# Optimization experiments

Hardware: AMD Instinct MI355X
Metric: run time of the kernel (lower is better)

Reference implementation:

```python
import jax, jax.numpy as jnp
import numpy as np

M0 = 0.5
M_MIN = 0.25
SCALE = 32.0
NUM_CLASSES = 100000
FEAT_DIM = 256
BATCH = 512


def setup_inputs() -> dict:
    key = jax.random.key(0)
    k1, k2, k3, k4 = jax.random.split(key, 4)
    features = jax.random.normal(k1, (BATCH, FEAT_DIM), dtype=jnp.float32)
    labels = jax.random.randint(k2, (BATCH,), 0, NUM_CLASSES, dtype=jnp.int64)
    weights = jax.random.uniform(k3, (BATCH,), dtype=jnp.float32)
    # xavier_uniform for (num_classes, feat_dim)
    limit = float(np.sqrt(6.0 / (NUM_CLASSES + FEAT_DIM)))
    weight = jax.random.uniform(k4, (NUM_CLASSES, FEAT_DIM), dtype=jnp.float32,
                                minval=-limit, maxval=limit)
    return {"features": features, "weight": weight, "weights": weights, "labels": labels}


def reference(features, weight, weights, labels):
    B = features.shape[0]
    norms = jnp.linalg.norm(features, axis=1)  # (B,)
    lo = jax.lax.stop_gradient(norms.min())
    hi = jax.lax.stop_gradient(norms.max())
    denom = jnp.maximum(hi - lo, 1e-8)
    margins = jnp.clip(M_MIN + (M0 - M_MIN) * (norms - lo) / denom, M_MIN, M0)  # (B,)

    feat_n = features / jnp.maximum(norms, 1e-12)[:, None]
    w_n = weight / jnp.maximum(jnp.linalg.norm(weight, axis=1), 1e-12)[:, None]
    cosine = jnp.clip(feat_n @ w_n.T, -1.0 + 1e-7, 1.0 - 1e-7)  # (B, C)

    rows = jnp.arange(B)
    cos_t = cosine[rows, labels]                      # target cosine (B,)
    theta_t = jnp.arccos(cos_t)
    cos_m_t = cos_t * jnp.cos(margins) - jnp.sin(theta_t) * jnp.sin(margins)

    logits = SCALE * cosine
    logits = logits.at[rows, labels].set(SCALE * cos_m_t)

    logp = jax.nn.log_softmax(logits, axis=1)
    per_sample = -logp[rows, labels]
    return (per_sample * weights).mean()
```

## Files before the change

kernel.cpp:

```cpp
#include <hip/hip_runtime.h>
#include <hip/hip_bf16.h>
#include <math.h>

#define BATCH 512
#define FEAT  256
#define NCLS  100000
#define SCALE_ 32.0f
#define M0_    0.5f
#define MMIN_  0.25f

#define BN 64
#define NT64 1563
#define NSLOTS 256
#define NPART 256
#define K4CHUNK 16
#define NK4 (NPART / K4CHUNK)

#define LOG2E_ 1.44269504088896f
#define K2C_   (SCALE_ * LOG2E_)

typedef unsigned short u16;
typedef short s16x8 __attribute__((ext_vector_type(8)));
typedef float f32x4 __attribute__((ext_vector_type(4)));

__device__ u16   g_fbf16[BATCH * FEAT];
__device__ float g_norms[BATCH];
__device__ float g_dot[BATCH];
__device__ float g_wn2[BATCH];
__device__ float g_psum[NPART * BATCH];
__device__ float g_qs[NK4 * BATCH];
__device__ int   g_lab32;

__device__ __forceinline__ u16 f2b(float x) {
  union { float f; unsigned u; } v; v.f = x;
  unsigned r = v.u + 0x7FFFu + ((v.u >> 16) & 1u);
  return (u16)(r >> 16);
}

__device__ __forceinline__ unsigned pkbf16(float a, float b) {
  unsigned r;
  asm("v_cvt_pk_bf16_f32 %0, %1, %2" : "=v"(r) : "v"(a), "v"(b));
  return r;
}

__device__ __forceinline__ float ex2(float x) {
  return __builtin_amdgcn_exp2f(x);
}

__global__ void k1a(const float* __restrict__ feat, const int* __restrict__ labw) {
  int wid = threadIdx.x >> 6, lane = threadIdx.x & 63;
  int row = blockIdx.x * 4 + wid;
  float4 f = ((const float4*)(feat + row * FEAT))[lane];
  float ss = f.x * f.x + f.y * f.y + f.z * f.z + f.w * f.w;
  #pragma unroll
  for (int d = 1; d < 64; d <<= 1) ss += __shfl_xor(ss, d, 64);
  float nrm = sqrtf(ss);
  float inv = 1.0f / fmaxf(nrm, 1e-12f);
  ushort4 h;
  h.x = f2b(f.x * inv); h.y = f2b(f.y * inv);
  h.z = f2b(f.z * inv); h.w = f2b(f.w * inv);
  ((ushort4*)(g_fbf16 + row * FEAT))[lane] = h;
  if (lane == 0) g_norms[row] = nrm;
  if (blockIdx.x == 0 && wid == 0) {
    int odd = 0;
    #pragma unroll
    for (int k = 0; k < 4; ++k) odd |= labw[2 * (k * 64 + lane) + 1];
    unsigned long long b = __ballot(odd != 0);
    if (lane == 0) g_lab32 = (b != 0ULL) ? 1 : 0;
  }
}

__global__ void k2c(const float* __restrict__ feat, const float* __restrict__ wmat,
                    const void* __restrict__ labels) {
  int wid = threadIdx.x >> 6, lane = threadIdx.x & 63;
  int i = blockIdx.x * 4 + wid;
  long long lab;
  if (g_lab32) lab = (long long)((const int*)labels)[i];
  else         lab = ((const long long*)labels)[i];
  float4 a = ((const float4*)(feat + i * FEAT))[lane];
  float4 b = ((const float4*)(wmat + (size_t)lab * FEAT))[lane];
  float d  = a.x * b.x + a.y * b.y + a.z * b.z + a.w * b.w;
  float bb = b.x * b.x + b.y * b.y + b.z * b.z + b.w * b.w;
  #pragma unroll
  for (int t = 1; t < 64; t <<= 1) {
    d  += __shfl_xor(d, t, 64);
    bb += __shfl_xor(bb, t, 64);
  }
  if (lane == 0) { g_dot[i] = d; g_wn2[i] = bb; }
}


#define LOADC(RB, TILE) do {                                                \
    rowL_ = (RB) + (tid >> 4);                                              \
    int rg_ = (TILE) * BN + rowL_; rg_ = rg_ < NCLS ? rg_ : NCLS - 1;       \
    const float4* src_ = (const float4*)(wmat + (size_t)rg_ * FEAT) + (tid & 15); \
    v_[0] = src_[0]; v_[1] = src_[16]; v_[2] = src_[32]; v_[3] = src_[48];  \
  } while (0)

#define FINISHC(NB) do {                                                    \
    float ss_ = 0.0f;                                                       \
    _Pragma("unroll")                                                       \
    for (int k_ = 0; k_ < 4; ++k_)                                          \
      ss_ += v_[k_].x * v_[k_].x + v_[k_].y * v_[k_].y                      \
           + v_[k_].z * v_[k_].z + v_[k_].w * v_[k_].w;                     \
    ss_ += __shfl_xor(ss_, 1, 64);                                          \
    ss_ += __shfl_xor(ss_, 2, 64);                                          \
    ss_ += __shfl_xor(ss_, 4, 64);                                          \
    ss_ += __shfl_xor(ss_, 8, 64);                                          \
    float inv_ = 1.0f / fmaxf(sqrtf(ss_), 1e-12f);                          \
    u16* dst_ = &Ws[NB][0] + rowL_ * FEAT;                                  \
    _Pragma("unroll")                                                       \
    for (int k_ = 0; k_ < 4; ++k_) {                                        \
      int p_ = (tid & 15) + k_ * 16;                                        \
      int2 w2_;                                                             \
      w2_.x = (int)pkbf16(v_[k_].x * inv_, v_[k_].y * inv_);                \
      w2_.y = (int)pkbf16(v_[k_].z * inv_, v_[k_].w * inv_);                \
      *(int2*)(dst_ + ((p_ >> 1) ^ (rowL_ & 7)) * 8 + (p_ & 1) * 4) = w2_;  \
    }                                                                       \
  } while (0)

#define PHASE(p8) do {                                                      \
    f32x4 acc[2];                                                           \
    acc[0] = f32x4{0.0f, 0.0f, 0.0f, 0.0f};                                 \
    acc[1] = f32x4{0.0f, 0.0f, 0.0f, 0.0f};                                 \
    const u16* wb = &Ws[buf][0];                                            \
    const int row_ = (p8) * 16 + s;                                         \
    _Pragma("unroll")                                                       \
    for (int c = 0; c < 8; ++c) {                                           \
      int cc = c * 4 + q;                                                   \
      s16x8 wf = *(const s16x8*)(wb + row_ * FEAT + (cc ^ (row_ & 7)) * 8); \
      acc[0] = __builtin_amdgcn_mfma_f32_16x16x32_bf16(wf, fr[0][c], acc[0], 0, 0, 0); \
      acc[1] = __builtin_amdgcn_mfma_f32_16x16x32_bf16(wf, fr[1][c], acc[1], 0, 0, 0); \
    }                                                                       \
    _Pragma("unroll")                                                       \
    for (int m = 0; m < 2; ++m) {                                           \
      float sl = 0.0f;                                                      \
      _Pragma("unroll")                                                     \
      for (int r = 0; r < 4; ++r) {                                         \
        float term = ex2(fmaf(acc[m][r], K2C_, -K2C_));                     \
        if (edge) {                                                         \
          int cls = tile * BN + (p8) * 16 + q * 4 + r;                      \
          if (cls >= NCLS) term = 0.0f;                                     \
        }                                                                   \
        sl += term;                                                         \
      }                                                                     \
      S[m] += sl;                                                           \
    }                                                                       \
  } while (0)

__global__ __launch_bounds__(512, 2) void k3(const float* __restrict__ wmat) {
  __shared__ __align__(16) u16 Ws[2][BN * FEAT];

  const int tid  = threadIdx.x;
  const int lane = tid & 63, wid = tid >> 6;
  const int s = lane & 15, q = lane >> 4;
  const int bid = blockIdx.x;
  const int nslot = bid & 255;
  const int sh = bid >> 8;
  const int niter = ((NT64 - 1 - nslot) >> 8) + 1;

  int rowL_;
  float4 v_[4];

  LOADC(0, nslot);  FINISHC(0);
  LOADC(32, nslot); FINISHC(0);

  s16x8 fr[2][8];
  {
    const int srow = sh * 256 + wid * 32;
    #pragma unroll
    for (int m = 0; m < 2; ++m)
      #pragma unroll
      for (int c = 0; c < 8; ++c)
        fr[m][c] = *(const s16x8*)(g_fbf16 + (srow + m * 16 + s) * FEAT + c * 32 + q * 8);
  }

  float S[2] = {0.0f, 0.0f};

  __syncthreads();

  int buf = 0;
  for (int t = 0; t < niter; ++t) {
    const int tile = nslot + t * NSLOTS;
    const bool last = (t + 1 == niter);
    const bool edge = (tile * BN + BN > NCLS);
    const int ntile = nslot + (t + 1) * NSLOTS;

    if (!last) LOADC(0, ntile);
    PHASE(0); PHASE(1);
    if (!last) { FINISHC(buf ^ 1); LOADC(32, ntile); }
    PHASE(2); PHASE(3);
    if (!last) FINISHC(buf ^ 1);
    __syncthreads();
    buf ^= 1;
  }

  #pragma unroll
  for (int m = 0; m < 2; ++m) {
    S[m] += __shfl_xor(S[m], 16, 64);
    S[m] += __shfl_xor(S[m], 32, 64);
  }

  if (lane < 16) {
    #pragma unroll
    for (int m = 0; m < 2; ++m) {
      int smp = sh * 256 + wid * 32 + m * 16 + lane;
      g_psum[nslot * BATCH + smp] = S[m];
    }
  }
}

__global__ __launch_bounds__(512) void k4a() {
  int i = threadIdx.x;
  int b = blockIdx.x;
  float S = 0.0f;
  #pragma unroll 4
  for (int p = b * K4CHUNK; p < b * K4CHUNK + K4CHUNK; ++p)
    S += g_psum[p * BATCH + i];
  g_qs[b * BATCH + i] = S;
}

__global__ void k4b(const float* __restrict__ wts, float* __restrict__ out) {
  int i = threadIdx.x;
  float S = 0.0f;
  #pragma unroll
  for (int t = 0; t < NK4; ++t) S += g_qs[t * BATCH + i];

  float n = g_norms[i];
  __shared__ float smin[512], smax[512];
  smin[i] = n; smax[i] = n;
  __syncthreads();
  for (int st = 256; st > 0; st >>= 1) {
    if (i < st) {
      smin[i] = fminf(smin[i], smin[i + st]);
      smax[i] = fmaxf(smax[i], smax[i + st]);
    }
    __syncthreads();
  }
  float lo = smin[0], hi = smax[0];
  float denom = fmaxf(hi - lo, 1e-8f);
  float mg = MMIN_ + (M0_ - MMIN_) * (n - lo) / denom;
  mg = fminf(fmaxf(mg, MMIN_), M0_);

  const float CLIP = 1.0f - 1e-7f;
  float wn = fmaxf(sqrtf(g_wn2[i]), 1e-12f);
  float ct = g_dot[i] / (fmaxf(n, 1e-12f) * wn);
  ct = fminf(fmaxf(ct, -CLIP), CLIP);

  float sint = sqrtf(fmaxf(0.0f, 1.0f - ct * ct));
  float cosm = ct * cosf(mg) - sint * sinf(mg);
  float b_old = K2C_ * ct;
  float b_new = K2C_ * cosm;
  float S2 = S - ex2(b_old - K2C_) + ex2(b_new - K2C_);
  float lse = 32.0f + logf(S2);
  float contrib = (lse - SCALE_ * cosm) * wts[i];
  __shared__ float sred[512];
  sred[i] = contrib;
  __syncthreads();
  for (int st = 256; st > 0; st >>= 1) {
    if (i < st) sred[i] += sred[i + st];
    __syncthreads();
  }
  if (i == 0) out[0] = sred[0] * (1.0f / (float)BATCH);
}

extern "C" void kernel_launch(void* const* d_in, const int* in_sizes, int n_in,
                              void* d_out, int out_size, void* d_ws, size_t ws_size,
                              hipStream_t stream) {
  const float* feat = (const float*)d_in[0];
  const float* wmat = (const float*)d_in[1];
  const float* wts  = (const float*)d_in[2];
  const void*  labs = d_in[3];
  float* out = (float*)d_out;

  hipLaunchKernelGGL(k1a, dim3(BATCH / 4), dim3(256), 0, stream, feat, (const int*)labs);
  hipLaunchKernelGGL(k2c, dim3(BATCH / 4), dim3(256), 0, stream, feat, wmat, labs);
  hipLaunchKernelGGL(k3,  dim3(512), dim3(512), 0, stream, wmat);
  hipLaunchKernelGGL(k4a, dim3(NK4), dim3(512), 0, stream);
  hipLaunchKernelGGL(k4b, dim3(1), dim3(512), 0, stream, wts, out);
}
```

Measured before the change: 61.06 us.

## Cover full batch per block with 128-class tiles to halve weight traffic

Each block of the main GEMM+softmax kernel now covers all 512 samples (64 per wave, four 16-row MFMA groups) and walks 128-class tiles, instead of two blocks each handling half the batch over 64-class tiles. Every weight row is therefore loaded, normalized and converted to bf16 only once rather than twice. The block count drops to 256 with one block per CU. The trade-offs are higher register pressure from 32 feature fragments and 4 accumulators, doubled LDS per block, and lower occupancy.

```diff
diff --git a/kernel.cpp b/kernel.cpp
--- a/kernel.cpp
+++ b/kernel.cpp
@@ -9,9 +9,9 @@
 #define M0_    0.5f
 #define MMIN_  0.25f
 
-#define BN 64
-#define NT64 1563
-#define NSLOTS 256
+#define BN 128
+#define NT 782
+#define NBLK 256
 #define NPART 256
 #define K4CHUNK 16
 #define NK4 (NPART / K4CHUNK)
@@ -91,49 +91,52 @@
 
 
 #define LOADC(RB, TILE) do {                                                \
-    rowL_ = (RB) + (tid >> 4);                                              \
+    rowL_ = (RB) + (tid >> 3);                                              \
     int rg_ = (TILE) * BN + rowL_; rg_ = rg_ < NCLS ? rg_ : NCLS - 1;       \
-    const float4* src_ = (const float4*)(wmat + (size_t)rg_ * FEAT) + (tid & 15); \
-    v_[0] = src_[0]; v_[1] = src_[16]; v_[2] = src_[32]; v_[3] = src_[48];  \
+    const float4* src_ = (const float4*)(wmat + (size_t)rg_ * FEAT) + (tid & 7) * 8; \
+    _Pragma("unroll")                                                       \
+    for (int k_ = 0; k_ < 8; ++k_) v_[k_] = src_[k_];                       \
   } while (0)
 
 #define FINISHC(NB) do {                                                    \
     float ss_ = 0.0f;                                                       \
     _Pragma("unroll")                                                       \
-    for (int k_ = 0; k_ < 4; ++k_)                                          \
+    for (int k_ = 0; k_ < 8; ++k_)                                          \
       ss_ += v_[k_].x * v_[k_].x + v_[k_].y * v_[k_].y                      \
            + v_[k_].z * v_[k_].z + v_[k_].w * v_[k_].w;                     \
     ss_ += __shfl_xor(ss_, 1, 64);                                          \
     ss_ += __shfl_xor(ss_, 2, 64);                                          \
     ss_ += __shfl_xor(ss_, 4, 64);                                          \
-    ss_ += __shfl_xor(ss_, 8, 64);                                          \
     float inv_ = 1.0f / fmaxf(sqrtf(ss_), 1e-12f);                          \
     u16* dst_ = &Ws[NB][0] + rowL_ * FEAT;                                  \
     _Pragma("unroll")                                                       \
     for (int k_ = 0; k_ < 4; ++k_) {                                        \
-      int p_ = (tid & 15) + k_ * 16;                                        \
-      int2 w2_;                                                             \
-      w2_.x = (int)pkbf16(v_[k_].x * inv_, v_[k_].y * inv_);                \
-      w2_.y = (int)pkbf16(v_[k_].z * inv_, v_[k_].w * inv_);                \
-      *(int2*)(dst_ + ((p_ >> 1) ^ (rowL_ & 7)) * 8 + (p_ & 1) * 4) = w2_;  \
+      int jj_ = (tid & 7) * 4 + k_;                                         \
+      int4 w4_;                                                             \
+      w4_.x = (int)pkbf16(v_[2*k_].x * inv_,   v_[2*k_].y * inv_);          \
+      w4_.y = (int)pkbf16(v_[2*k_].z * inv_,   v_[2*k_].w * inv_);          \
+      w4_.z = (int)pkbf16(v_[2*k_+1].x * inv_, v_[2*k_+1].y * inv_);        \
+      w4_.w = (int)pkbf16(v_[2*k_+1].z * inv_, v_[2*k_+1].w * inv_);        \
+      *(int4*)(dst_ + ((jj_ ^ (rowL_ & 7)) * 8)) = w4_;                     \
     }                                                                       \
   } while (0)
 
 #define PHASE(p8) do {                                                      \
-    f32x4 acc[2];                                                           \
-    acc[0] = f32x4{0.0f, 0.0f, 0.0f, 0.0f};                                 \
-    acc[1] = f32x4{0.0f, 0.0f, 0.0f, 0.0f};                                 \
+    f32x4 acc[4];                                                           \
+    _Pragma("unroll")                                                       \
+    for (int m = 0; m < 4; ++m) acc[m] = f32x4{0.0f, 0.0f, 0.0f, 0.0f};     \
     const u16* wb = &Ws[buf][0];                                            \
     const int row_ = (p8) * 16 + s;                                         \
     _Pragma("unroll")                                                       \
     for (int c = 0; c < 8; ++c) {                                           \
       int cc = c * 4 + q;                                                   \
       s16x8 wf = *(const s16x8*)(wb + row_ * FEAT + (cc ^ (row_ & 7)) * 8); \
-      acc[0] = __builtin_amdgcn_mfma_f32_16x16x32_bf16(wf, fr[0][c], acc[0], 0, 0, 0); \
-      acc[1] = __builtin_amdgcn_mfma_f32_16x16x32_bf16(wf, fr[1][c], acc[1], 0, 0, 0); \
+      _Pragma("unroll")                                                     \
+      for (int m = 0; m < 4; ++m)                                           \
+        acc[m] = __builtin_amdgcn_mfma_f32_16x16x32_bf16(wf, fr[m][c], acc[m], 0, 0, 0); \
     }                                                                       \
     _Pragma("unroll")                                                       \
-    for (int m = 0; m < 2; ++m) {                                           \
+    for (int m = 0; m < 4; ++m) {                                           \
       float sl = 0.0f;                                                      \
       _Pragma("unroll")                                                     \
       for (int r = 0; r < 4; ++r) {                                         \
@@ -148,64 +151,62 @@
     }                                                                       \
   } while (0)
 
-__global__ __launch_bounds__(512, 2) void k3(const float* __restrict__ wmat) {
+__global__ __launch_bounds__(512, 1) void k3(const float* __restrict__ wmat) {
   __shared__ __align__(16) u16 Ws[2][BN * FEAT];
 
   const int tid  = threadIdx.x;
   const int lane = tid & 63, wid = tid >> 6;
   const int s = lane & 15, q = lane >> 4;
   const int bid = blockIdx.x;
-  const int nslot = bid & 255;
-  const int sh = bid >> 8;
-  const int niter = ((NT64 - 1 - nslot) >> 8) + 1;
+  const int niter = (bid < (NT - 3 * NBLK)) ? 4 : 3;
 
   int rowL_;
-  float4 v_[4];
-
-  LOADC(0, nslot);  FINISHC(0);
-  LOADC(32, nslot); FINISHC(0);
-
-  s16x8 fr[2][8];
+  float4 v_[8];
+
+  LOADC(0, bid);  FINISHC(0);
+  LOADC(64, bid); FINISHC(0);
+
+  s16x8 fr[4][8];
   {
-    const int srow = sh * 256 + wid * 32;
+    const int srow = wid * 64;
     #pragma unroll
-    for (int m = 0; m < 2; ++m)
+    for (int m = 0; m < 4; ++m)
       #pragma unroll
       for (int c = 0; c < 8; ++c)
         fr[m][c] = *(const s16x8*)(g_fbf16 + (srow + m * 16 + s) * FEAT + c * 32 + q * 8);
   }
 
-  float S[2] = {0.0f, 0.0f};
+  float S[4] = {0.0f, 0.0f, 0.0f, 0.0f};
 
   __syncthreads();
 
   int buf = 0;
   for (int t = 0; t < niter; ++t) {
-    const int tile = nslot + t * NSLOTS;
+    const int tile = bid + t * NBLK;
     const bool last = (t + 1 == niter);
     const bool edge = (tile * BN + BN > NCLS);
-    const int ntile = nslot + (t + 1) * NSLOTS;
+    const int ntile = bid + (t + 1) * NBLK;
 
     if (!last) LOADC(0, ntile);
-    PHASE(0); PHASE(1);
-    if (!last) { FINISHC(buf ^ 1); LOADC(32, ntile); }
-    PHASE(2); PHASE(3);
+    PHASE(0); PHASE(1); PHASE(2); PHASE(3);
+    if (!last) { FINISHC(buf ^ 1); LOADC(64, ntile); }
+    PHASE(4); PHASE(5); PHASE(6); PHASE(7);
     if (!last) FINISHC(buf ^ 1);
     __syncthreads();
     buf ^= 1;
   }
 
   #pragma unroll
-  for (int m = 0; m < 2; ++m) {
+  for (int m = 0; m < 4; ++m) {
     S[m] += __shfl_xor(S[m], 16, 64);
     S[m] += __shfl_xor(S[m], 32, 64);
   }
 
   if (lane < 16) {
     #pragma unroll
-    for (int m = 0; m < 2; ++m) {
-      int smp = sh * 256 + wid * 32 + m * 16 + lane;
-      g_psum[nslot * BATCH + smp] = S[m];
+    for (int m = 0; m < 4; ++m) {
+      int smp = wid * 64 + m * 16 + lane;
+      g_psum[bid * BATCH + smp] = S[m];
     }
   }
 }
@@ -275,7 +276,7 @@
 
   hipLaunchKernelGGL(k1a, dim3(BATCH / 4), dim3(256), 0, stream, feat, (const int*)labs);
   hipLaunchKernelGGL(k2c, dim3(BATCH / 4), dim3(256), 0, stream, feat, wmat, labs);
-  hipLaunchKernelGGL(k3,  dim3(512), dim3(512), 0, stream, wmat);
+  hipLaunchKernelGGL(k3,  dim3(NBLK), dim3(512), 0, stream, wmat);
   hipLaunchKernelGGL(k4a, dim3(NK4), dim3(512), 0, stream);
   hipLaunchKernelGGL(k4b, dim3(1), dim3(512), 0, stream, wts, out);
 }
```

New measurement: 101.8 us. 1.67x slower.

## Halve class tile to 32 rows, drop edge masking, widen LDS stores

Applied to the files above, without the earlier changes.

Shrinks the class tile from 64 to 32 rows. Because 100000 divides evenly by 32, the per-element edge masking and row clamping can be removed. Each thread now loads four contiguous float4s and writes 16-byte LDS stores instead of 8-byte ones, and the loop runs twice as many iterations with one load and finish step between two MFMA phases. The aim is to cut masking overhead and LDS store count, and the shared buffers shrink too, at the cost of more iterations and more barriers per tile of work.

```diff
diff --git a/kernel.cpp b/kernel.cpp
--- a/kernel.cpp
+++ b/kernel.cpp
@@ -9,8 +9,8 @@
 #define M0_    0.5f
 #define MMIN_  0.25f
 
-#define BN 64
-#define NT64 1563
+#define BN 32
+#define NT32 3125
 #define NSLOTS 256
 #define NPART 256
 #define K4CHUNK 16
@@ -90,11 +90,11 @@
 }
 
 
-#define LOADC(RB, TILE) do {                                                \
-    rowL_ = (RB) + (tid >> 4);                                              \
-    int rg_ = (TILE) * BN + rowL_; rg_ = rg_ < NCLS ? rg_ : NCLS - 1;       \
-    const float4* src_ = (const float4*)(wmat + (size_t)rg_ * FEAT) + (tid & 15); \
-    v_[0] = src_[0]; v_[1] = src_[16]; v_[2] = src_[32]; v_[3] = src_[48];  \
+#define LOADC(TILE) do {                                                    \
+    rowL_ = tid >> 4;                                                       \
+    int rg_ = (TILE) * BN + rowL_;                                          \
+    const float4* src_ = (const float4*)(wmat + (size_t)rg_ * FEAT + (tid & 15) * 16); \
+    v_[0] = src_[0]; v_[1] = src_[1]; v_[2] = src_[2]; v_[3] = src_[3];     \
   } while (0)
 
 #define FINISHC(NB) do {                                                    \
@@ -110,12 +110,14 @@
     float inv_ = 1.0f / fmaxf(sqrtf(ss_), 1e-12f);                          \
     u16* dst_ = &Ws[NB][0] + rowL_ * FEAT;                                  \
     _Pragma("unroll")                                                       \
-    for (int k_ = 0; k_ < 4; ++k_) {                                        \
-      int p_ = (tid & 15) + k_ * 16;                                        \
-      int2 w2_;                                                             \
-      w2_.x = (int)pkbf16(v_[k_].x * inv_, v_[k_].y * inv_);                \
-      w2_.y = (int)pkbf16(v_[k_].z * inv_, v_[k_].w * inv_);                \
-      *(int2*)(dst_ + ((p_ >> 1) ^ (rowL_ & 7)) * 8 + (p_ & 1) * 4) = w2_;  \
+    for (int k_ = 0; k_ < 2; ++k_) {                                        \
+      int jj_ = (tid & 15) * 2 + k_;                                        \
+      int4 w4_;                                                             \
+      w4_.x = (int)pkbf16(v_[2*k_].x * inv_,   v_[2*k_].y * inv_);          \
+      w4_.y = (int)pkbf16(v_[2*k_].z * inv_,   v_[2*k_].w * inv_);          \
+      w4_.z = (int)pkbf16(v_[2*k_+1].x * inv_, v_[2*k_+1].y * inv_);        \
+      w4_.w = (int)pkbf16(v_[2*k_+1].z * inv_, v_[2*k_+1].w * inv_);        \
+      *(int4*)(dst_ + ((jj_ ^ (rowL_ & 7)) * 8)) = w4_;                     \
     }                                                                       \
   } while (0)
 
@@ -134,16 +136,10 @@
     }                                                                       \
     _Pragma("unroll")                                                       \
     for (int m = 0; m < 2; ++m) {                                           \
-      float sl = 0.0f;                                                      \
-      _Pragma("unroll")                                                     \
-      for (int r = 0; r < 4; ++r) {                                         \
-        float term = ex2(fmaf(acc[m][r], K2C_, -K2C_));                     \
-        if (edge) {                                                         \
-          int cls = tile * BN + (p8) * 16 + q * 4 + r;                      \
-          if (cls >= NCLS) term = 0.0f;                                     \
-        }                                                                   \
-        sl += term;                                                         \
-      }                                                                     \
+      float sl = ex2(fmaf(acc[m][0], K2C_, -K2C_))                          \
+               + ex2(fmaf(acc[m][1], K2C_, -K2C_))                          \
+               + ex2(fmaf(acc[m][2], K2C_, -K2C_))                          \
+               + ex2(fmaf(acc[m][3], K2C_, -K2C_));                         \
       S[m] += sl;                                                           \
     }                                                                       \
   } while (0)
@@ -157,13 +153,12 @@
   const int bid = blockIdx.x;
   const int nslot = bid & 255;
   const int sh = bid >> 8;
-  const int niter = ((NT64 - 1 - nslot) >> 8) + 1;
+  const int niter = ((NT32 - 1 - nslot) >> 8) + 1;
 
   int rowL_;
   float4 v_[4];
 
-  LOADC(0, nslot);  FINISHC(0);
-  LOADC(32, nslot); FINISHC(0);
+  LOADC(nslot); FINISHC(0);
 
   s16x8 fr[2][8];
   {
@@ -181,16 +176,12 @@
 
   int buf = 0;
   for (int t = 0; t < niter; ++t) {
-    const int tile = nslot + t * NSLOTS;
     const bool last = (t + 1 == niter);
-    const bool edge = (tile * BN + BN > NCLS);
-    const int ntile = nslot + (t + 1) * NSLOTS;
-
-    if (!last) LOADC(0, ntile);
-    PHASE(0); PHASE(1);
-    if (!last) { FINISHC(buf ^ 1); LOADC(32, ntile); }
-    PHASE(2); PHASE(3);
+
+    if (!last) LOADC(nslot + (t + 1) * NSLOTS);
+    PHASE(0);
     if (!last) FINISHC(buf ^ 1);
+    PHASE(1);
     __syncthreads();
     buf ^= 1;
   }
```

After: 60.11 us. Within noise of the previous version (-1.6%).
